# Kernel tuning notes

Hardware: AMD Instinct MI355X
Metric: run time of the kernel (lower is better)

## Reference

```python
import jax, jax.numpy as jnp
import numpy as np

B, L, D, H, DEPTH = 64, 384, 128, 8, 6
DH = D // H          # 16
VOCAB = 32000
C_OUT = 128
FF = 4 * D           # reformer_pytorch default ff_mult=4
SELF_VAL = -5e4      # TOKEN_SELF_ATTN_VALUE
MASK_VAL = -1e9      # causal mask value


def layer_norm(x, g, b, eps=1e-5):
    mu = jnp.mean(x, -1, keepdims=True)
    var = jnp.mean((x - mu) ** 2, -1, keepdims=True)
    return (x - mu) * jax.lax.rsqrt(var + eps) * g + b


def attn_block(x, p):
    # PreNorm + LSHSelfAttention in full-QK-attention fallback (seq <= full_attn_thres)
    h = layer_norm(x, p['ln1_g'], p['ln1_b'])
    qk = (h @ p['Wqk']).reshape(B, L, H, DH).transpose(0, 2, 1, 3)  # [B,H,L,DH]
    v = (h @ p['Wv']).reshape(B, L, H, DH).transpose(0, 2, 1, 3)
    # shared QK: q = qk, k = l2-normalized qk
    k = qk / jnp.maximum(jnp.linalg.norm(qk, axis=-1, keepdims=True), 1e-12)
    dots = jnp.einsum('bhid,bhjd->bhij', qk, k) * (DH ** -0.5)
    i = jnp.arange(L)
    eye = i[:, None] == i[None, :]
    future = i[None, :] > i[:, None]
    dots = jnp.where(eye, SELF_VAL, dots)   # token cannot (easily) attend to itself
    dots = jnp.where(future, MASK_VAL, dots)  # causal
    a = jax.nn.softmax(dots, axis=-1)
    o = jnp.einsum('bhij,bhjd->bhid', a, v).transpose(0, 2, 1, 3).reshape(B, L, D)
    return o @ p['Wo'] + p['bo']


def ff_block(x, p):
    h = layer_norm(x, p['ln2_g'], p['ln2_b'])
    h = jax.nn.gelu(h @ p['W1'] + p['b1'], approximate=False)
    return h @ p['W2'] + p['b2']


def forward(x_enc, emb, pos1, pos2, ln1_g, ln1_b, Wqk, Wv, Wo, bo,
            ln2_g, ln2_b, W1, b1, W2, b2, lnf_g, lnf_b, Wp, bp):
    # axial positional embedding (summed mode): (25,D) + (25,D) -> (625,D)
    pos = (pos1[:, None, :] + pos2[None, :, :]).reshape(25 * 25, D)[:L]
    x = emb[x_enc] + pos  # [B,L,D]

    layer_params = dict(ln1_g=ln1_g, ln1_b=ln1_b, Wqk=Wqk, Wv=Wv, Wo=Wo, bo=bo,
                        ln2_g=ln2_g, ln2_b=ln2_b, W1=W1, b1=b1, W2=W2, b2=b2)

    def block(carry, p):
        x1, x2 = carry
        y1 = x1 + attn_block(x2, p)
        y2 = x2 + ff_block(y1, p)
        return (y1, y2), None

    # reversible-net math: duplicate stream, run blocks, average the two halves
    (x1, x2), _ = jax.lax.scan(block, (x, x), layer_params)
    x = layer_norm((x1 + x2) * 0.5, lnf_g, lnf_b)
    return x.reshape(B, L * D) @ Wp + bp  # [B, C_OUT]


def setup_inputs() -> dict:
    key = jax.random.key(0)
    ks = jax.random.split(key, 12)
    s = 0.02
    inp = {
        'x_enc': jax.random.randint(ks[0], (B, L), 0, VOCAB, dtype=jnp.int32),
        'emb': jax.random.normal(ks[1], (VOCAB, D), jnp.float32) * s,
        'pos1': jax.random.normal(ks[2], (25, D), jnp.float32) * s,
        'pos2': jax.random.normal(ks[3], (25, D), jnp.float32) * s,
        'ln1_g': jnp.ones((DEPTH, D), jnp.float32),
        'ln1_b': jnp.zeros((DEPTH, D), jnp.float32),
        'Wqk': jax.random.normal(ks[4], (DEPTH, D, D), jnp.float32) * s,
        'Wv': jax.random.normal(ks[5], (DEPTH, D, D), jnp.float32) * s,
        'Wo': jax.random.normal(ks[6], (DEPTH, D, D), jnp.float32) * s,
        'bo': jnp.zeros((DEPTH, D), jnp.float32),
        'ln2_g': jnp.ones((DEPTH, D), jnp.float32),
        'ln2_b': jnp.zeros((DEPTH, D), jnp.float32),
        'W1': jax.random.normal(ks[7], (DEPTH, D, FF), jnp.float32) * s,
        'b1': jnp.zeros((DEPTH, FF), jnp.float32),
        'W2': jax.random.normal(ks[8], (DEPTH, FF, D), jnp.float32) * s,
        'b2': jnp.zeros((DEPTH, D), jnp.float32),
        'lnf_g': jnp.ones((D,), jnp.float32),
        'lnf_b': jnp.zeros((D,), jnp.float32),
        'Wp': jax.random.normal(ks[9], (L * D, C_OUT), jnp.float32) * s,
        'bp': jnp.zeros((C_OUT,), jnp.float32),
    }
    return inp


def reference(x_enc, emb, pos1, pos2, ln1_g, ln1_b, Wqk, Wv, Wo, bo,
              ln2_g, ln2_b, W1, b1, W2, b2, lnf_g, lnf_b, Wp, bp):
    return forward(x_enc, emb, pos1, pos2, ln1_g, ln1_b, Wqk, Wv, Wo, bo,
                   ln2_g, ln2_b, W1, b1, W2, b2, lnf_g, lnf_b, Wp, bp)
```

## Files before the change

### kernel.cpp

```cpp
#include <hip/hip_runtime.h>
#include <hip/hip_bf16.h>
#include <math.h>

#define BB 64
#define LL 384
#define DD 128
#define HH 8
#define DHH 16
#define DEPTH 6
#define FFD 512
#define MROWS (BB*LL)
#define COUT 128
#define KP (LL*DD)
#define KSPLIT 96
#define KCHUNK 512

typedef short bf16x8 __attribute__((ext_vector_type(8)));
typedef float f32x4 __attribute__((ext_vector_type(4)));

__device__ __forceinline__ unsigned short f2bs(float x) {
    __hip_bfloat16 h = __float2bfloat16(x);
    return *reinterpret_cast<unsigned short*>(&h);
}
__device__ __forceinline__ float bs2f(unsigned short u) {
    unsigned int v = ((unsigned int)u) << 16;
    return __uint_as_float(v);
}
__device__ __forceinline__ float gelu_exact(float x) {
    return 0.5f * x * (1.0f + erff(x * 0.70710678118654752f));
}

__global__ __launch_bounds__(256) void embedln_kernel(
    const int* __restrict__ x_enc, const float* __restrict__ emb,
    const float* __restrict__ pos1, const float* __restrict__ pos2,
    const float* __restrict__ g, const float* __restrict__ b,
    float* __restrict__ x1, float* __restrict__ x2,
    __hip_bfloat16* __restrict__ y)
{
    int wave = threadIdx.x >> 6;
    int lane = threadIdx.x & 63;
    int row = blockIdx.x * 4 + wave;
    int l = row % LL;
    int tok = x_enc[row];
    float2 e  = ((const float2*)(emb + (size_t)tok * DD))[lane];
    float2 p1 = ((const float2*)(pos1 + (l / 25) * DD))[lane];
    float2 p2 = ((const float2*)(pos2 + (l % 25) * DD))[lane];
    float2 v = make_float2(e.x + p1.x + p2.x, e.y + p1.y + p2.y);
    ((float2*)(x1 + (size_t)row * DD))[lane] = v;
    ((float2*)(x2 + (size_t)row * DD))[lane] = v;
    float2 gg = ((const float2*)g)[lane];
    float2 bb = ((const float2*)b)[lane];
    float s = v.x + v.y;
    float sq = v.x * v.x + v.y * v.y;
    #pragma unroll
    for (int off = 32; off > 0; off >>= 1) {
        s += __shfl_down(s, off, 64);
        sq += __shfl_down(sq, off, 64);
    }
    s = __shfl(s, 0, 64);
    sq = __shfl(sq, 0, 64);
    float mean = s * (1.0f / DD);
    float var = sq * (1.0f / DD) - mean * mean;
    float rstd = rsqrtf(var + 1e-5f);
    __hip_bfloat16* yp = y + (size_t)row * DD + lane * 2;
    yp[0] = __float2bfloat16((v.x - mean) * rstd * gg.x + bb.x);
    yp[1] = __float2bfloat16((v.y - mean) * rstd * gg.y + bb.y);
}

__device__ __forceinline__ void castT_body(
    const float* __restrict__ s, __hip_bfloat16* __restrict__ d,
    int K, int N, int kb, int nb)
{
    __shared__ float tile[32][33];
    int tx = threadIdx.x & 31, ty = threadIdx.x >> 5;
    #pragma unroll
    for (int r = 0; r < 32; r += 8)
        tile[r + ty][tx] = s[(size_t)(kb + r + ty) * N + nb + tx];
    __syncthreads();
    #pragma unroll
    for (int r = 0; r < 32; r += 8)
        d[(size_t)(nb + r + ty) * K + kb + tx] = __float2bfloat16(tile[tx][r + ty]);
}

__global__ __launch_bounds__(256) void cast_all_kernel(
    const float* __restrict__ Wqk, const float* __restrict__ Wv,
    const float* __restrict__ Wo,  const float* __restrict__ W1,
    const float* __restrict__ W2,
    __hip_bfloat16* __restrict__ dqk, __hip_bfloat16* __restrict__ dv,
    __hip_bfloat16* __restrict__ dwo, __hip_bfloat16* __restrict__ d1,
    __hip_bfloat16* __restrict__ d2)
{
    int z = blockIdx.x;
    if (z < 288) {
        int m = z >> 4, t = z & 15;
        int which = m / 6, dd = m % 6;
        const float* s = (which == 0 ? Wqk : (which == 1 ? Wv : Wo)) + (size_t)dd * 16384;
        __hip_bfloat16* d = (which == 0 ? dqk : (which == 1 ? dv : dwo))
                            + (size_t)dd * (which == 2 ? 16384 : 32768);
        castT_body(s, d, 128, 128, (t >> 2) * 32, (t & 3) * 32);
    } else if (z < 672) {
        int i = z - 288; int dd = i >> 6; int t = i & 63;
        castT_body(W1 + (size_t)dd * 65536, d1 + (size_t)dd * 65536,
                   128, 512, (t >> 4) * 32, (t & 15) * 32);
    } else {
        int i = z - 672; int dd = i >> 6; int t = i & 63;
        castT_body(W2 + (size_t)dd * 65536, d2 + (size_t)dd * 65536,
                   512, 128, (t >> 2) * 32, (t & 3) * 32);
    }
}

__global__ __launch_bounds__(256) void castWp_kernel(
    const float* __restrict__ src, __hip_bfloat16* __restrict__ dst)
{
    castT_body(src, dst, KP, 128, blockIdx.x * 32, blockIdx.y * 32);
}

template<int K, int N>
__global__ __launch_bounds__(256) void gemm_qkv_kernel(
    const __hip_bfloat16* __restrict__ A, const __hip_bfloat16* __restrict__ Bt,
    __hip_bfloat16* __restrict__ Cdst)
{
    __shared__ unsigned short As[64 * 128];
    __shared__ unsigned short Bs[128 * 128];
    int tid = threadIdx.x;
    int l = tid & 63, w = tid >> 6;
    int wr = w >> 1, wc = w & 1;
    int lr = l & 15, q = l >> 4;
    int m0 = blockIdx.y * 64;
    int n0 = blockIdx.x * 128;

    f32x4 acc[2][4];
    #pragma unroll
    for (int mt = 0; mt < 2; ++mt)
        #pragma unroll
        for (int nt = 0; nt < 4; ++nt) acc[mt][nt] = (f32x4){0.f, 0.f, 0.f, 0.f};

    for (int kt = 0; kt < K; kt += 128) {
        if (kt) __syncthreads();
        #pragma unroll
        for (int p = 0; p < 4; ++p) {
            int n = p * 256 + tid;
            int r = n >> 4;
            int c = (n & 15) ^ (r & 7);
            *(uint4*)&As[n * 8] = *(const uint4*)(A + (size_t)(m0 + r) * K + kt + c * 8);
        }
        #pragma unroll
        for (int p = 0; p < 8; ++p) {
            int n = p * 256 + tid;
            int r = n >> 4;
            int c = (n & 15) ^ (r & 7);
            *(uint4*)&Bs[n * 8] = *(const uint4*)(Bt + (size_t)(n0 + r) * K + kt + c * 8);
        }
        __syncthreads();
        #pragma unroll
        for (int kk = 0; kk < 4; ++kk) {
            bf16x8 afr[2], bfr[4];
            #pragma unroll
            for (int mt = 0; mt < 2; ++mt) {
                int rA = wr * 32 + mt * 16 + lr;
                int cc = (kk * 4 + q) ^ (rA & 7);
                afr[mt] = *(const bf16x8*)&As[(rA * 16 + cc) * 8];
            }
            #pragma unroll
            for (int nt = 0; nt < 4; ++nt) {
                int rB = wc * 64 + nt * 16 + lr;
                int cc = (kk * 4 + q) ^ (rB & 7);
                bfr[nt] = *(const bf16x8*)&Bs[(rB * 16 + cc) * 8];
            }
            #pragma unroll
            for (int mt = 0; mt < 2; ++mt)
                #pragma unroll
                for (int nt = 0; nt < 4; ++nt)
                    acc[mt][nt] = __builtin_amdgcn_mfma_f32_16x16x32_bf16(
                        afr[mt], bfr[nt], acc[mt][nt], 0, 0, 0);
        }
    }

    #pragma unroll
    for (int mt = 0; mt < 2; ++mt)
        #pragma unroll
        for (int nt = 0; nt < 4; ++nt) {
            int col = n0 + wc * 64 + nt * 16 + lr;
            #pragma unroll
            for (int r = 0; r < 4; ++r) {
                int row = m0 + wr * 32 + mt * 16 + q * 4 + r;
                Cdst[(size_t)row * N + col] = __float2bfloat16(acc[mt][nt][r]);
            }
        }
}

__global__ __launch_bounds__(256) void attn_kernel(
    const __hip_bfloat16* __restrict__ qkv, __hip_bfloat16* __restrict__ o)
{
    int z  = blockIdx.x >> 9;
    int bh = blockIdx.x & 511;
    int b = bh >> 3, hh = bh & 7;
    const unsigned short* base = (const unsigned short*)qkv + (size_t)b * LL * 256 + hh * DHH;

    __shared__ unsigned short knb[LL + 2][24];
    __shared__ unsigned short vtb[16][LL + 24];
    __shared__ float cq[LL];
    __shared__ unsigned short ptile[4][16][40];

    int t = threadIdx.x;
    for (int r = t; r < LL; r += 256) {
        const unsigned short* qp = base + (size_t)r * 256;
        unsigned short qs[16], vs16[16];
        *(uint4*)&qs[0]  = *(const uint4*)(qp);
        *(uint4*)&qs[8]  = *(const uint4*)(qp + 8);
        *(uint4*)&vs16[0] = *(const uint4*)(qp + 128);
        *(uint4*)&vs16[8] = *(const uint4*)(qp + 136);
        float q[16];
        #pragma unroll
        for (int d = 0; d < 16; ++d) q[d] = bs2f(qs[d]);
        float nrm = 0.f;
        #pragma unroll
        for (int d = 0; d < 16; ++d) nrm = fmaf(q[d], q[d], nrm);
        float qn = sqrtf(nrm);
        float inv = 1.0f / fmaxf(qn, 1e-12f);
        cq[r] = 0.25f * qn;
        unsigned short kb[16];
        #pragma unroll
        for (int d = 0; d < 16; ++d) kb[d] = f2bs(q[d] * inv);
        *(uint4*)&knb[r][0] = *(uint4*)&kb[0];
        *(uint4*)&knb[r][8] = *(uint4*)&kb[8];
        *(uint4*)&knb[r][16] = make_uint4(0u, 0u, 0u, 0u);
        #pragma unroll
        for (int d = 0; d < 16; ++d) vtb[d][r] = vs16[d];
    }
    if (t < 16) {
        #pragma unroll
        for (int c = 0; c < 24; ++c) vtb[t][LL + c] = 0;
    }
    if (t < 2) {
        #pragma unroll
        for (int c = 0; c < 24; ++c) knb[LL + t][c] = 0;
    }

    int w = t >> 6, l = t & 63;
    int lr = l & 15, q4 = l >> 4;
    __syncthreads();

    bf16x8 zfrag = {0, 0, 0, 0, 0, 0, 0, 0};
    bf16x8 onesf;
    #pragma unroll
    for (int i = 0; i < 8; ++i) onesf[i] = (short)0x3F80;

    int slot = 2 * w + z;
    int strips[3] = { slot, 15 - slot, 16 + slot };
    #pragma unroll
    for (int si = 0; si < 3; ++si) {
        int s = strips[si];
        int r0 = s * 16;
        bf16x8 bq = *(const bf16x8*)&knb[r0 + lr][q4 * 8];
        float ccq = cq[r0 + lr];
        int qg = r0 + lr;

        f32x4 oacc = (f32x4){0.f, 0.f, 0.f, 0.f};
        f32x4 lacc = (f32x4){0.f, 0.f, 0.f, 0.f};

        for (int jt = 0; jt <= s; jt += 2) {
            bf16x8 a0 = *(const bf16x8*)&knb[jt * 16 + lr][(q4 & 1) * 8];
            a0 = (q4 < 2) ? a0 : zfrag;
            bf16x8 a1 = *(const bf16x8*)&knb[(jt + 1) * 16 + lr][(q4 & 1) * 8];
            a1 = (q4 < 2) ? a1 : zfrag;
            f32x4 s0 = __builtin_amdgcn_mfma_f32_16x16x32_bf16(
                a0, bq, (f32x4){0.f, 0.f, 0.f, 0.f}, 0, 0, 0);
            f32x4 s1 = __builtin_amdgcn_mfma_f32_16x16x32_bf16(
                a1, bq, (f32x4){0.f, 0.f, 0.f, 0.f}, 0, 0, 0);

            unsigned int pk0[2], pk1[2];
            #pragma unroll
            for (int h = 0; h < 2; ++h) {
                int ja = jt * 16 + q4 * 4 + 2 * h;
                float pa = __expf(fmaf(s0[2 * h],     ccq, -ccq));
                pa = (ja < qg) ? pa : 0.f;
                float pb = __expf(fmaf(s0[2 * h + 1], ccq, -ccq));
                pb = (ja + 1 < qg) ? pb : 0.f;
                pk0[h] = (unsigned int)f2bs(pa) | ((unsigned int)f2bs(pb) << 16);
                float pc = __expf(fmaf(s1[2 * h],     ccq, -ccq));
                pc = (ja + 16 < qg) ? pc : 0.f;
                float pd = __expf(fmaf(s1[2 * h + 1], ccq, -ccq));
                pd = (ja + 17 < qg) ? pd : 0.f;
                pk1[h] = (unsigned int)f2bs(pc) | ((unsigned int)f2bs(pd) << 16);
            }
            *(uint2*)&ptile[w][lr][q4 * 4]      = make_uint2(pk0[0], pk0[1]);
            *(uint2*)&ptile[w][lr][16 + q4 * 4] = make_uint2(pk1[0], pk1[1]);
            asm volatile("s_waitcnt lgkmcnt(0)" ::: "memory");
            bf16x8 pfrag = *(const bf16x8*)&ptile[w][lr][q4 * 8];
            bf16x8 vfrag = *(const bf16x8*)&vtb[lr][jt * 16 + q4 * 8];
            oacc = __builtin_amdgcn_mfma_f32_16x16x32_bf16(pfrag, vfrag, oacc, 0, 0, 0);
            lacc = __builtin_amdgcn_mfma_f32_16x16x32_bf16(pfrag, onesf, lacc, 0, 0, 0);
        }

        if (s == 0 && q4 == 0) {
            lacc[0] = 1.0f;
            oacc[0] = bs2f(vtb[lr][0]);
        }
        unsigned short* ob = (unsigned short*)o + (size_t)(b * LL + r0) * DD + hh * 16 + lr;
        #pragma unroll
        for (int reg = 0; reg < 4; ++reg) {
            float ov = oacc[reg] / lacc[reg];
            ob[(size_t)(q4 * 4 + reg) * DD] = f2bs(ov);
        }
    }
}

__global__ __launch_bounds__(256) void mega_wolf_kernel(
    const __hip_bfloat16* __restrict__ Ao, const __hip_bfloat16* __restrict__ WoTd,
    const float* __restrict__ bod, float* __restrict__ x1,
    const float* __restrict__ lng, const float* __restrict__ lnb,
    const __hip_bfloat16* __restrict__ W1Td, const float* __restrict__ b1d,
    __hip_bfloat16* __restrict__ hff)
{
    __shared__ unsigned short As[32 * 128];
    __shared__ unsigned short Bs[128 * 128];
    int tid = threadIdx.x;
    int l = tid & 63, w = tid >> 6;
    int lr = l & 15, q = l >> 4;
    int m0 = blockIdx.x * 32;

    f32x4 acc[2][2];
    #pragma unroll
    for (int mt = 0; mt < 2; ++mt)
        #pragma unroll
        for (int nt = 0; nt < 2; ++nt) acc[mt][nt] = (f32x4){0.f, 0.f, 0.f, 0.f};

    #pragma unroll
    for (int p = 0; p < 2; ++p) {
        int n = p * 256 + tid;
        int r = n >> 4;
        int c = (n & 15) ^ (r & 7);
        *(uint4*)&As[n * 8] = *(const uint4*)(Ao + (size_t)(m0 + r) * 128 + c * 8);
    }
    #pragma unroll
    for (int p = 0; p < 8; ++p) {
        int n = p * 256 + tid;
        int r = n >> 4;
        int c = (n & 15) ^ (r & 7);
        *(uint4*)&Bs[n * 8] = *(const uint4*)(WoTd + (size_t)r * 128 + c * 8);
    }
    __syncthreads();
    #pragma unroll
    for (int kk = 0; kk < 4; ++kk) {
        bf16x8 afr[2], bfr[2];
        #pragma unroll
        for (int mt = 0; mt < 2; ++mt) {
            int rA = mt * 16 + lr;
            int cc = (kk * 4 + q) ^ (rA & 7);
            afr[mt] = *(const bf16x8*)&As[(rA * 16 + cc) * 8];
        }
        #pragma unroll
        for (int nt = 0; nt < 2; ++nt) {
            int rB = w * 32 + nt * 16 + lr;
            int cc = (kk * 4 + q) ^ (rB & 7);
            bfr[nt] = *(const bf16x8*)&Bs[(rB * 16 + cc) * 8];
        }
        #pragma unroll
        for (int mt = 0; mt < 2; ++mt)
            #pragma unroll
            for (int nt = 0; nt < 2; ++nt)
                acc[mt][nt] = __builtin_amdgcn_mfma_f32_16x16x32_bf16(
                    afr[mt], bfr[nt], acc[mt][nt], 0, 0, 0);
    }

    float* fp = (float*)Bs;
    __syncthreads();
    #pragma unroll
    for (int mt = 0; mt < 2; ++mt)
        #pragma unroll
        for (int nt = 0; nt < 2; ++nt) {
            int col = w * 32 + nt * 16 + lr;
            float bv = bod[col];
            #pragma unroll
            for (int r = 0; r < 4; ++r) {
                int rowL = mt * 16 + q * 4 + r;
                fp[rowL * 128 + col] = acc[mt][nt][r] + bv
                                       + x1[(size_t)(m0 + rowL) * 128 + col];
            }
        }
    __syncthreads();
    {
        int rl = tid >> 3, sub = tid & 7;
        float s = 0.f, sq = 0.f;
        #pragma unroll
        for (int c4 = 0; c4 < 4; ++c4) {
            float4 v = *(const float4*)&fp[rl * 128 + sub * 16 + c4 * 4];
            s  += (v.x + v.y) + (v.z + v.w);
            sq += (v.x * v.x + v.y * v.y) + (v.z * v.z + v.w * v.w);
        }
        s  += __shfl_xor(s, 1);  s  += __shfl_xor(s, 2);  s  += __shfl_xor(s, 4);
        sq += __shfl_xor(sq, 1); sq += __shfl_xor(sq, 2); sq += __shfl_xor(sq, 4);
        float mean = s * (1.0f / 128.0f);
        float var  = sq * (1.0f / 128.0f) - mean * mean;
        float rstd = rsqrtf(var + 1e-5f);
        #pragma unroll
        for (int c4 = 0; c4 < 4; ++c4) {
            int col = sub * 16 + c4 * 4;
            float4 v  = *(const float4*)&fp[rl * 128 + col];
            *(float4*)(x1 + (size_t)(m0 + rl) * 128 + col) = v;
            float4 g4 = *(const float4*)(lng + col);
            float4 b4 = *(const float4*)(lnb + col);
            unsigned short pk[4];
            pk[0] = f2bs((v.x - mean) * rstd * g4.x + b4.x);
            pk[1] = f2bs((v.y - mean) * rstd * g4.y + b4.y);
            pk[2] = f2bs((v.z - mean) * rstd * g4.z + b4.z);
            pk[3] = f2bs((v.w - mean) * rstd * g4.w + b4.w);
            int addr = rl * 128 + (((col >> 3) ^ (rl & 7)) << 3) + (col & 7);
            *(ushort4*)&As[addr] = *(ushort4*)&pk[0];
        }
    }
    __syncthreads();

    for (int nc = 0; nc < 4; ++nc) {
        if (nc) __syncthreads();
        #pragma unroll
        for (int p = 0; p < 8; ++p) {
            int n = p * 256 + tid;
            int r = n >> 4;
            int c = (n & 15) ^ (r & 7);
            *(uint4*)&Bs[n * 8] = *(const uint4*)(W1Td + (size_t)(nc * 128 + r) * 128 + c * 8);
        }
        __syncthreads();
        f32x4 a2[2][2];
        #pragma unroll
        for (int mt = 0; mt < 2; ++mt)
            #pragma unroll
            for (int nt = 0; nt < 2; ++nt) a2[mt][nt] = (f32x4){0.f, 0.f, 0.f, 0.f};
        #pragma unroll
        for (int kk = 0; kk < 4; ++kk) {
            bf16x8 afr[2], bfr[2];
            #pragma unroll
            for (int mt = 0; mt < 2; ++mt) {
                int rA = mt * 16 + lr;
                int cc = (kk * 4 + q) ^ (rA & 7);
                afr[mt] = *(const bf16x8*)&As[(rA * 16 + cc) * 8];
            }
            #pragma unroll
            for (int nt = 0; nt < 2; ++nt) {
                int rB = w * 32 + nt * 16 + lr;
                int cc = (kk * 4 + q) ^ (rB & 7);
                bfr[nt] = *(const bf16x8*)&Bs[(rB * 16 + cc) * 8];
            }
            #pragma unroll
            for (int mt = 0; mt < 2; ++mt)
                #pragma unroll
                for (int nt = 0; nt < 2; ++nt)
                    a2[mt][nt] = __builtin_amdgcn_mfma_f32_16x16x32_bf16(
                        afr[mt], bfr[nt], a2[mt][nt], 0, 0, 0);
        }
        #pragma unroll
        for (int mt = 0; mt < 2; ++mt)
            #pragma unroll
            for (int nt = 0; nt < 2; ++nt) {
                int colg = nc * 128 + w * 32 + nt * 16 + lr;
                float bv = b1d[colg];
                #pragma unroll
                for (int r = 0; r < 4; ++r) {
                    int row = m0 + mt * 16 + q * 4 + r;
                    hff[(size_t)row * 512 + colg] =
                        __float2bfloat16(gelu_exact(a2[mt][nt][r] + bv));
                }
            }
    }
}

template<bool LAST>
__global__ __launch_bounds__(256) void mega_ffq_kernel(
    const __hip_bfloat16* __restrict__ Ahff, const __hip_bfloat16* __restrict__ W2Td,
    const float* __restrict__ b2d, float* __restrict__ x2,
    const float* __restrict__ x1,
    const float* __restrict__ lng, const float* __restrict__ lnb,
    const __hip_bfloat16* __restrict__ WqvTd, __hip_bfloat16* __restrict__ qkv,
    __hip_bfloat16* __restrict__ hout)
{
    __shared__ unsigned short As[32 * 128];
    __shared__ unsigned short Bs[128 * 128];
    int tid = threadIdx.x;
    int l = tid & 63, w = tid >> 6;
    int lr = l & 15, q = l >> 4;
    int m0 = blockIdx.x * 32;

    f32x4 acc[2][2];
    #pragma unroll
    for (int mt = 0; mt < 2; ++mt)
        #pragma unroll
        for (int nt = 0; nt < 2; ++nt) acc[mt][nt] = (f32x4){0.f, 0.f, 0.f, 0.f};

    for (int kt = 0; kt < 512; kt += 128) {
        if (kt) __syncthreads();
        #pragma unroll
        for (int p = 0; p < 2; ++p) {
            int n = p * 256 + tid;
            int r = n >> 4;
            int c = (n & 15) ^ (r & 7);
            *(uint4*)&As[n * 8] = *(const uint4*)(Ahff + (size_t)(m0 + r) * 512 + kt + c * 8);
        }
        #pragma unroll
        for (int p = 0; p < 8; ++p) {
            int n = p * 256 + tid;
            int r = n >> 4;
            int c = (n & 15) ^ (r & 7);
            *(uint4*)&Bs[n * 8] = *(const uint4*)(W2Td + (size_t)r * 512 + kt + c * 8);
        }
        __syncthreads();
        #pragma unroll
        for (int kk = 0; kk < 4; ++kk) {
            bf16x8 afr[2], bfr[2];
            #pragma unroll
            for (int mt = 0; mt < 2; ++mt) {
                int rA = mt * 16 + lr;
                int cc = (kk * 4 + q) ^ (rA & 7);
                afr[mt] = *(const bf16x8*)&As[(rA * 16 + cc) * 8];
            }
            #pragma unroll
            for (int nt = 0; nt < 2; ++nt) {
                int rB = w * 32 + nt * 16 + lr;
                int cc = (kk * 4 + q) ^ (rB & 7);
                bfr[nt] = *(const bf16x8*)&Bs[(rB * 16 + cc) * 8];
            }
            #pragma unroll
            for (int mt = 0; mt < 2; ++mt)
                #pragma unroll
                for (int nt = 0; nt < 2; ++nt)
                    acc[mt][nt] = __builtin_amdgcn_mfma_f32_16x16x32_bf16(
                        afr[mt], bfr[nt], acc[mt][nt], 0, 0, 0);
        }
    }

    float* fp = (float*)Bs;
    __syncthreads();
    #pragma unroll
    for (int mt = 0; mt < 2; ++mt)
        #pragma unroll
        for (int nt = 0; nt < 2; ++nt) {
            int col = w * 32 + nt * 16 + lr;
            float bv = b2d[col];
            #pragma unroll
            for (int r = 0; r < 4; ++r) {
                int rowL = mt * 16 + q * 4 + r;
                fp[rowL * 128 + col] = acc[mt][nt][r] + bv
                                       + x2[(size_t)(m0 + rowL) * 128 + col];
            }
        }
    __syncthreads();
    {
        int rl = tid >> 3, sub = tid & 7;
        float s = 0.f, sq = 0.f;
        #pragma unroll
        for (int c4 = 0; c4 < 4; ++c4) {
            float4 v = *(const float4*)&fp[rl * 128 + sub * 16 + c4 * 4];
            if (LAST) {
                float4 xo = *(const float4*)(x1 + (size_t)(m0 + rl) * 128 + sub * 16 + c4 * 4);
                v.x = (v.x + xo.x) * 0.5f; v.y = (v.y + xo.y) * 0.5f;
                v.z = (v.z + xo.z) * 0.5f; v.w = (v.w + xo.w) * 0.5f;
            }
            s  += (v.x + v.y) + (v.z + v.w);
            sq += (v.x * v.x + v.y * v.y) + (v.z * v.z + v.w * v.w);
        }
        s  += __shfl_xor(s, 1);  s  += __shfl_xor(s, 2);  s  += __shfl_xor(s, 4);
        sq += __shfl_xor(sq, 1); sq += __shfl_xor(sq, 2); sq += __shfl_xor(sq, 4);
        float mean = s * (1.0f / 128.0f);
        float var  = sq * (1.0f / 128.0f) - mean * mean;
        float rstd = rsqrtf(var + 1e-5f);
        #pragma unroll
        for (int c4 = 0; c4 < 4; ++c4) {
            int col = sub * 16 + c4 * 4;
            float4 v = *(const float4*)&fp[rl * 128 + col];
            if (LAST) {
                float4 xo = *(const float4*)(x1 + (size_t)(m0 + rl) * 128 + col);
                v.x = (v.x + xo.x) * 0.5f; v.y = (v.y + xo.y) * 0.5f;
                v.z = (v.z + xo.z) * 0.5f; v.w = (v.w + xo.w) * 0.5f;
            } else {
                *(float4*)(x2 + (size_t)(m0 + rl) * 128 + col) = v;
            }
            float4 g4 = *(const float4*)(lng + col);
            float4 b4 = *(const float4*)(lnb + col);
            unsigned short pk[4];
            pk[0] = f2bs((v.x - mean) * rstd * g4.x + b4.x);
            pk[1] = f2bs((v.y - mean) * rstd * g4.y + b4.y);
            pk[2] = f2bs((v.z - mean) * rstd * g4.z + b4.z);
            pk[3] = f2bs((v.w - mean) * rstd * g4.w + b4.w);
            if (LAST) {
                *(ushort4*)((unsigned short*)hout + (size_t)(m0 + rl) * 128 + col)
                    = *(ushort4*)&pk[0];
            } else {
                int addr = rl * 128 + (((col >> 3) ^ (rl & 7)) << 3) + (col & 7);
                *(ushort4*)&As[addr] = *(ushort4*)&pk[0];
            }
        }
    }
    __syncthreads();

    if (!LAST) {
        for (int nc = 0; nc < 2; ++nc) {
            if (nc) __syncthreads();
            #pragma unroll
            for (int p = 0; p < 8; ++p) {
                int n = p * 256 + tid;
                int r = n >> 4;
                int c = (n & 15) ^ (r & 7);
                *(uint4*)&Bs[n * 8] = *(const uint4*)(WqvTd + (size_t)(nc * 128 + r) * 128 + c * 8);
            }
            __syncthreads();
            f32x4 a2[2][2];
            #pragma unroll
            for (int mt = 0; mt < 2; ++mt)
                #pragma unroll
                for (int nt = 0; nt < 2; ++nt) a2[mt][nt] = (f32x4){0.f, 0.f, 0.f, 0.f};
            #pragma unroll
            for (int kk = 0; kk < 4; ++kk) {
                bf16x8 afr[2], bfr[2];
                #pragma unroll
                for (int mt = 0; mt < 2; ++mt) {
                    int rA = mt * 16 + lr;
                    int cc = (kk * 4 + q) ^ (rA & 7);
                    afr[mt] = *(const bf16x8*)&As[(rA * 16 + cc) * 8];
                }
                #pragma unroll
                for (int nt = 0; nt < 2; ++nt) {
                    int rB = w * 32 + nt * 16 + lr;
                    int cc = (kk * 4 + q) ^ (rB & 7);
                    bfr[nt] = *(const bf16x8*)&Bs[(rB * 16 + cc) * 8];
                }
                #pragma unroll
                for (int mt = 0; mt < 2; ++mt)
                    #pragma unroll
                    for (int nt = 0; nt < 2; ++nt)
                        a2[mt][nt] = __builtin_amdgcn_mfma_f32_16x16x32_bf16(
                            afr[mt], bfr[nt], a2[mt][nt], 0, 0, 0);
            }
            #pragma unroll
            for (int mt = 0; mt < 2; ++mt)
                #pragma unroll
                for (int nt = 0; nt < 2; ++nt) {
                    int colg = nc * 128 + w * 32 + nt * 16 + lr;
                    #pragma unroll
                    for (int r = 0; r < 4; ++r) {
                        int row = m0 + mt * 16 + q * 4 + r;
                        qkv[(size_t)row * 256 + colg] = __float2bfloat16(a2[mt][nt][r]);
                    }
                }
        }
    }
}

__global__ __launch_bounds__(256) void final_mfma_kernel(
    const __hip_bfloat16* __restrict__ A, const __hip_bfloat16* __restrict__ Bt,
    float* __restrict__ partials)
{
    __shared__ unsigned short As[64 * 128];
    __shared__ unsigned short Bs[128 * 128];
    int tid = threadIdx.x;
    int l = tid & 63, w = tid >> 6;
    int wr = w >> 1, wc = w & 1;
    int lr = l & 15, q = l >> 4;
    int kbase = blockIdx.x * KCHUNK;

    f32x4 acc[2][4];
    #pragma unroll
    for (int mt = 0; mt < 2; ++mt)
        #pragma unroll
        for (int nt = 0; nt < 4; ++nt) acc[mt][nt] = (f32x4){0.f, 0.f, 0.f, 0.f};

    for (int kt = 0; kt < KCHUNK; kt += 128) {
        if (kt) __syncthreads();
        #pragma unroll
        for (int p = 0; p < 4; ++p) {
            int n = p * 256 + tid;
            int r = n >> 4;
            int c = (n & 15) ^ (r & 7);
            *(uint4*)&As[n * 8] = *(const uint4*)(A + (size_t)r * KP + kbase + kt + c * 8);
        }
        #pragma unroll
        for (int p = 0; p < 8; ++p) {
            int n = p * 256 + tid;
            int r = n >> 4;
            int c = (n & 15) ^ (r & 7);
            *(uint4*)&Bs[n * 8] = *(const uint4*)(Bt + (size_t)r * KP + kbase + kt + c * 8);
        }
        __syncthreads();
        #pragma unroll
        for (int kk = 0; kk < 4; ++kk) {
            bf16x8 afr[2], bfr[4];
            #pragma unroll
            for (int mt = 0; mt < 2; ++mt) {
                int rA = wr * 32 + mt * 16 + lr;
                int cc = (kk * 4 + q) ^ (rA & 7);
                afr[mt] = *(const bf16x8*)&As[(rA * 16 + cc) * 8];
            }
            #pragma unroll
            for (int nt = 0; nt < 4; ++nt) {
                int rB = wc * 64 + nt * 16 + lr;
                int cc = (kk * 4 + q) ^ (rB & 7);
                bfr[nt] = *(const bf16x8*)&Bs[(rB * 16 + cc) * 8];
            }
            #pragma unroll
            for (int mt = 0; mt < 2; ++mt)
                #pragma unroll
                for (int nt = 0; nt < 4; ++nt)
                    acc[mt][nt] = __builtin_amdgcn_mfma_f32_16x16x32_bf16(
                        afr[mt], bfr[nt], acc[mt][nt], 0, 0, 0);
        }
    }

    float* dst = partials + (size_t)blockIdx.x * (64 * 128);
    #pragma unroll
    for (int mt = 0; mt < 2; ++mt)
        #pragma unroll
        for (int nt = 0; nt < 4; ++nt) {
            int col = wc * 64 + nt * 16 + lr;
            #pragma unroll
            for (int r = 0; r < 4; ++r) {
                int row = wr * 32 + mt * 16 + q * 4 + r;
                dst[row * 128 + col] = acc[mt][nt][r];
            }
        }
}

__global__ __launch_bounds__(256) void final_reduce_kernel(
    const float* __restrict__ partials, const float* __restrict__ bp,
    float* __restrict__ out)
{
    int j = blockIdx.x * 256 + threadIdx.x;
    float s = bp[j & (COUT - 1)];
    #pragma unroll 8
    for (int p = 0; p < KSPLIT; ++p)
        s += partials[(size_t)p * 8192 + j];
    out[j] = s;
}

extern "C" void kernel_launch(void* const* d_in, const int* in_sizes, int n_in,
                              void* d_out, int out_size, void* d_ws, size_t ws_size,
                              hipStream_t stream)
{
    const int*   x_enc = (const int*)  d_in[0];
    const float* emb   = (const float*)d_in[1];
    const float* pos1  = (const float*)d_in[2];
    const float* pos2  = (const float*)d_in[3];
    const float* ln1_g = (const float*)d_in[4];
    const float* ln1_b = (const float*)d_in[5];
    const float* Wqk   = (const float*)d_in[6];
    const float* Wv    = (const float*)d_in[7];
    const float* Wo    = (const float*)d_in[8];
    const float* bo    = (const float*)d_in[9];
    const float* ln2_g = (const float*)d_in[10];
    const float* ln2_b = (const float*)d_in[11];
    const float* W1    = (const float*)d_in[12];
    const float* b1    = (const float*)d_in[13];
    const float* W2    = (const float*)d_in[14];
    const float* b2    = (const float*)d_in[15];
    const float* lnf_g = (const float*)d_in[16];
    const float* lnf_b = (const float*)d_in[17];
    const float* Wp    = (const float*)d_in[18];
    const float* bp    = (const float*)d_in[19];
    float* out = (float*)d_out;

    const size_t SZ = (size_t)MROWS * DD;
    float* ws_f = (float*)d_ws;
    float* x1 = ws_f;
    float* x2 = ws_f + SZ;
    __hip_bfloat16* hff  = (__hip_bfloat16*)(ws_f + 2 * SZ);
    __hip_bfloat16* h_bf = (__hip_bfloat16*)(ws_f + 4 * SZ);
    __hip_bfloat16* o_bf = h_bf + SZ;
    __hip_bfloat16* wqvT = o_bf + SZ;
    __hip_bfloat16* woT  = wqvT + 6 * 32768;
    __hip_bfloat16* w1T  = woT  + 6 * 16384;
    __hip_bfloat16* w2T  = w1T  + 6 * 65536;
    __hip_bfloat16* WpT  = w2T  + 6 * 65536;
    __hip_bfloat16* qkv  = WpT;
    float* partials = (float*)(WpT + (size_t)COUT * KP);

    cast_all_kernel<<<dim3(1056), dim3(256), 0, stream>>>(
        Wqk, Wv, Wo, W1, W2, wqvT, wqvT + 16384, woT, w1T, w2T);
    embedln_kernel<<<dim3(MROWS / 4), dim3(256), 0, stream>>>(
        x_enc, emb, pos1, pos2, ln1_g, ln1_b, x1, x2, h_bf);
    gemm_qkv_kernel<128, 256><<<dim3(2, MROWS / 64), dim3(256), 0, stream>>>(
        h_bf, wqvT, qkv);

    for (int d = 0; d < DEPTH; ++d) {
        attn_kernel<<<dim3(BB * HH * 2), dim3(256), 0, stream>>>(qkv, o_bf);
        mega_wolf_kernel<<<dim3(MROWS / 32), dim3(256), 0, stream>>>(
            o_bf, woT + (size_t)d * 16384, bo + d * DD, x1,
            ln2_g + d * DD, ln2_b + d * DD,
            w1T + (size_t)d * 65536, b1 + d * FFD, hff);
        if (d < DEPTH - 1) {
            mega_ffq_kernel<false><<<dim3(MROWS / 32), dim3(256), 0, stream>>>(
                hff, w2T + (size_t)d * 65536, b2 + d * DD, x2, nullptr,
                ln1_g + (d + 1) * DD, ln1_b + (d + 1) * DD,
                wqvT + (size_t)(d + 1) * 32768, qkv, nullptr);
        } else {
            mega_ffq_kernel<true><<<dim3(MROWS / 32), dim3(256), 0, stream>>>(
                hff, w2T + (size_t)d * 65536, b2 + d * DD, x2, x1,
                lnf_g, lnf_b, nullptr, nullptr, h_bf);
        }
    }

    castWp_kernel<<<dim3(KP / 32, 4), dim3(256), 0, stream>>>(Wp, WpT);
    final_mfma_kernel<<<dim3(KSPLIT), dim3(256), 0, stream>>>(h_bf, WpT, partials);
    final_reduce_kernel<<<dim3(32), dim3(256), 0, stream>>>(partials, bp, out);
}
```

Measured before the change: 555.0 us.

## Fuse FF1-GELU-FF2 and next-layer QKV into single per-layer kernel

Merges the Wo+LN2+W1+GELU kernel with the W2+residual+LN1+QKV kernel. The 512-wide GELU activation for a 32-row tile now lives in shared memory one 128-column chunk at a time, and W2 partial products accumulate in registers. This removes the global write and re-read of the large bf16 hff buffer and one launch per layer. In exchange it adds an extra shared-memory buffer, which may lower occupancy, and more barriers inside the chunk loop.

```diff
diff --git a/kernel.cpp b/kernel.cpp
--- a/kernel.cpp
+++ b/kernel.cpp
@@ -306,15 +306,21 @@
     }
 }
 
-__global__ __launch_bounds__(256) void mega_wolf_kernel(
+template<bool LAST>
+__global__ __launch_bounds__(256) void mega_layer_kernel(
     const __hip_bfloat16* __restrict__ Ao, const __hip_bfloat16* __restrict__ WoTd,
     const float* __restrict__ bod, float* __restrict__ x1,
-    const float* __restrict__ lng, const float* __restrict__ lnb,
+    const float* __restrict__ ln2g, const float* __restrict__ ln2b,
     const __hip_bfloat16* __restrict__ W1Td, const float* __restrict__ b1d,
-    __hip_bfloat16* __restrict__ hff)
+    const __hip_bfloat16* __restrict__ W2Td, const float* __restrict__ b2d,
+    float* __restrict__ x2,
+    const float* __restrict__ ln1g, const float* __restrict__ ln1b,
+    const __hip_bfloat16* __restrict__ WqvTd, __hip_bfloat16* __restrict__ qkv,
+    __hip_bfloat16* __restrict__ hout)
 {
     __shared__ unsigned short As[32 * 128];
     __shared__ unsigned short Bs[128 * 128];
+    __shared__ unsigned short Hs[32 * 128];
     int tid = threadIdx.x;
     int l = tid & 63, w = tid >> 6;
     int lr = l & 15, q = l >> 4;
@@ -399,18 +405,24 @@
             int col = sub * 16 + c4 * 4;
             float4 v  = *(const float4*)&fp[rl * 128 + col];
             *(float4*)(x1 + (size_t)(m0 + rl) * 128 + col) = v;
-            float4 g4 = *(const float4*)(lng + col);
-            float4 b4 = *(const float4*)(lnb + col);
+            float4 g4 = *(const float4*)(ln2g + col);
+            float4 b4 = *(const float4*)(ln2b + col);
             unsigned short pk[4];
             pk[0] = f2bs((v.x - mean) * rstd * g4.x + b4.x);
             pk[1] = f2bs((v.y - mean) * rstd * g4.y + b4.y);
             pk[2] = f2bs((v.z - mean) * rstd * g4.z + b4.z);
             pk[3] = f2bs((v.w - mean) * rstd * g4.w + b4.w);
             int addr = rl * 128 + (((col >> 3) ^ (rl & 7)) << 3) + (col & 7);
-            *(ushort4*)&As[addr] = *(ushort4*)&pk[0];
-        }
-    }
-    __syncthreads();
+            *(ushort4*)&Hs[addr] = *(ushort4*)&pk[0];
+        }
+    }
+    __syncthreads();
+
+    f32x4 ffacc[2][2];
+    #pragma unroll
+    for (int mt = 0; mt < 2; ++mt)
+        #pragma unroll
+        for (int nt = 0; nt < 2; ++nt) ffacc[mt][nt] = (f32x4){0.f, 0.f, 0.f, 0.f};
 
     for (int nc = 0; nc < 4; ++nc) {
         if (nc) __syncthreads();
@@ -422,11 +434,55 @@
             *(uint4*)&Bs[n * 8] = *(const uint4*)(W1Td + (size_t)(nc * 128 + r) * 128 + c * 8);
         }
         __syncthreads();
-        f32x4 a2[2][2];
+        f32x4 a1[2][2];
         #pragma unroll
         for (int mt = 0; mt < 2; ++mt)
             #pragma unroll
-            for (int nt = 0; nt < 2; ++nt) a2[mt][nt] = (f32x4){0.f, 0.f, 0.f, 0.f};
+            for (int nt = 0; nt < 2; ++nt) a1[mt][nt] = (f32x4){0.f, 0.f, 0.f, 0.f};
+        #pragma unroll
+        for (int kk = 0; kk < 4; ++kk) {
+            bf16x8 afr[2], bfr[2];
+            #pragma unroll
+            for (int mt = 0; mt < 2; ++mt) {
+                int rA = mt * 16 + lr;
+                int cc = (kk * 4 + q) ^ (rA & 7);
+                afr[mt] = *(const bf16x8*)&Hs[(rA * 16 + cc) * 8];
+            }
+            #pragma unroll
+            for (int nt = 0; nt < 2; ++nt) {
+                int rB = w * 32 + nt * 16 + lr;
+                int cc = (kk * 4 + q) ^ (rB & 7);
+                bfr[nt] = *(const bf16x8*)&Bs[(rB * 16 + cc) * 8];
+            }
+            #pragma unroll
+            for (int mt = 0; mt < 2; ++mt)
+                #pragma unroll
+                for (int nt = 0; nt < 2; ++nt)
+                    a1[mt][nt] = __builtin_amdgcn_mfma_f32_16x16x32_bf16(
+                        afr[mt], bfr[nt], a1[mt][nt], 0, 0, 0);
+        }
+        #pragma unroll
+        for (int mt = 0; mt < 2; ++mt)
+            #pragma unroll
+            for (int nt = 0; nt < 2; ++nt) {
+                int k = w * 32 + nt * 16 + lr;
+                float bv = b1d[nc * 128 + k];
+                #pragma unroll
+                for (int r = 0; r < 4; ++r) {
+                    int row = mt * 16 + q * 4 + r;
+                    int addr = row * 128 + (((k >> 3) ^ (row & 7)) << 3) + (k & 7);
+                    As[addr] = f2bs(gelu_exact(a1[mt][nt][r] + bv));
+                }
+            }
+        __syncthreads();
+        #pragma unroll
+        for (int p = 0; p < 8; ++p) {
+            int n = p * 256 + tid;
+            int r = n >> 4;
+            int c = (n & 15) ^ (r & 7);
+            *(uint4*)&Bs[n * 8] = *(const uint4*)(W2Td + (size_t)r * 512 + nc * 128 + c * 8);
+        }
+        __syncthreads();
         #pragma unroll
         for (int kk = 0; kk < 4; ++kk) {
             bf16x8 afr[2], bfr[2];
@@ -446,89 +502,11 @@
             for (int mt = 0; mt < 2; ++mt)
                 #pragma unroll
                 for (int nt = 0; nt < 2; ++nt)
-                    a2[mt][nt] = __builtin_amdgcn_mfma_f32_16x16x32_bf16(
-                        afr[mt], bfr[nt], a2[mt][nt], 0, 0, 0);
-        }
-        #pragma unroll
-        for (int mt = 0; mt < 2; ++mt)
-            #pragma unroll
-            for (int nt = 0; nt < 2; ++nt) {
-                int colg = nc * 128 + w * 32 + nt * 16 + lr;
-                float bv = b1d[colg];
-                #pragma unroll
-                for (int r = 0; r < 4; ++r) {
-                    int row = m0 + mt * 16 + q * 4 + r;
-                    hff[(size_t)row * 512 + colg] =
-                        __float2bfloat16(gelu_exact(a2[mt][nt][r] + bv));
-                }
-            }
-    }
-}
-
-template<bool LAST>
-__global__ __launch_bounds__(256) void mega_ffq_kernel(
-    const __hip_bfloat16* __restrict__ Ahff, const __hip_bfloat16* __restrict__ W2Td,
-    const float* __restrict__ b2d, float* __restrict__ x2,
-    const float* __restrict__ x1,
-    const float* __restrict__ lng, const float* __restrict__ lnb,
-    const __hip_bfloat16* __restrict__ WqvTd, __hip_bfloat16* __restrict__ qkv,
-    __hip_bfloat16* __restrict__ hout)
-{
-    __shared__ unsigned short As[32 * 128];
-    __shared__ unsigned short Bs[128 * 128];
-    int tid = threadIdx.x;
-    int l = tid & 63, w = tid >> 6;
-    int lr = l & 15, q = l >> 4;
-    int m0 = blockIdx.x * 32;
-
-    f32x4 acc[2][2];
-    #pragma unroll
-    for (int mt = 0; mt < 2; ++mt)
-        #pragma unroll
-        for (int nt = 0; nt < 2; ++nt) acc[mt][nt] = (f32x4){0.f, 0.f, 0.f, 0.f};
-
-    for (int kt = 0; kt < 512; kt += 128) {
-        if (kt) __syncthreads();
-        #pragma unroll
-        for (int p = 0; p < 2; ++p) {
-            int n = p * 256 + tid;
-            int r = n >> 4;
-            int c = (n & 15) ^ (r & 7);
-            *(uint4*)&As[n * 8] = *(const uint4*)(Ahff + (size_t)(m0 + r) * 512 + kt + c * 8);
-        }
-        #pragma unroll
-        for (int p = 0; p < 8; ++p) {
-            int n = p * 256 + tid;
-            int r = n >> 4;
-            int c = (n & 15) ^ (r & 7);
-            *(uint4*)&Bs[n * 8] = *(const uint4*)(W2Td + (size_t)r * 512 + kt + c * 8);
-        }
-        __syncthreads();
-        #pragma unroll
-        for (int kk = 0; kk < 4; ++kk) {
-            bf16x8 afr[2], bfr[2];
-            #pragma unroll
-            for (int mt = 0; mt < 2; ++mt) {
-                int rA = mt * 16 + lr;
-                int cc = (kk * 4 + q) ^ (rA & 7);
-                afr[mt] = *(const bf16x8*)&As[(rA * 16 + cc) * 8];
-            }
-            #pragma unroll
-            for (int nt = 0; nt < 2; ++nt) {
-                int rB = w * 32 + nt * 16 + lr;
-                int cc = (kk * 4 + q) ^ (rB & 7);
-                bfr[nt] = *(const bf16x8*)&Bs[(rB * 16 + cc) * 8];
-            }
-            #pragma unroll
-            for (int mt = 0; mt < 2; ++mt)
-                #pragma unroll
-                for (int nt = 0; nt < 2; ++nt)
-                    acc[mt][nt] = __builtin_amdgcn_mfma_f32_16x16x32_bf16(
-                        afr[mt], bfr[nt], acc[mt][nt], 0, 0, 0);
-        }
-    }
-
-    float* fp = (float*)Bs;
+                    ffacc[mt][nt] = __builtin_amdgcn_mfma_f32_16x16x32_bf16(
+                        afr[mt], bfr[nt], ffacc[mt][nt], 0, 0, 0);
+        }
+    }
+
     __syncthreads();
     #pragma unroll
     for (int mt = 0; mt < 2; ++mt)
@@ -539,7 +517,7 @@
             #pragma unroll
             for (int r = 0; r < 4; ++r) {
                 int rowL = mt * 16 + q * 4 + r;
-                fp[rowL * 128 + col] = acc[mt][nt][r] + bv
+                fp[rowL * 128 + col] = ffacc[mt][nt][r] + bv
                                        + x2[(size_t)(m0 + rowL) * 128 + col];
             }
         }
@@ -574,8 +552,8 @@
             } else {
                 *(float4*)(x2 + (size_t)(m0 + rl) * 128 + col) = v;
             }
-            float4 g4 = *(const float4*)(lng + col);
-            float4 b4 = *(const float4*)(lnb + col);
+            float4 g4 = *(const float4*)(ln1g + col);
+            float4 b4 = *(const float4*)(ln1b + col);
             unsigned short pk[4];
             pk[0] = f2bs((v.x - mean) * rstd * g4.x + b4.x);
             pk[1] = f2bs((v.y - mean) * rstd * g4.y + b4.y);
@@ -586,7 +564,7 @@
                     = *(ushort4*)&pk[0];
             } else {
                 int addr = rl * 128 + (((col >> 3) ^ (rl & 7)) << 3) + (col & 7);
-                *(ushort4*)&As[addr] = *(ushort4*)&pk[0];
+                *(ushort4*)&Hs[addr] = *(ushort4*)&pk[0];
             }
         }
     }
@@ -615,7 +593,7 @@
                 for (int mt = 0; mt < 2; ++mt) {
                     int rA = mt * 16 + lr;
                     int cc = (kk * 4 + q) ^ (rA & 7);
-                    afr[mt] = *(const bf16x8*)&As[(rA * 16 + cc) * 8];
+                    afr[mt] = *(const bf16x8*)&Hs[(rA * 16 + cc) * 8];
                 }
                 #pragma unroll
                 for (int nt = 0; nt < 2; ++nt) {
@@ -760,8 +738,7 @@
     float* ws_f = (float*)d_ws;
     float* x1 = ws_f;
     float* x2 = ws_f + SZ;
-    __hip_bfloat16* hff  = (__hip_bfloat16*)(ws_f + 2 * SZ);
-    __hip_bfloat16* h_bf = (__hip_bfloat16*)(ws_f + 4 * SZ);
+    __hip_bfloat16* h_bf = (__hip_bfloat16*)(ws_f + 2 * SZ);
     __hip_bfloat16* o_bf = h_bf + SZ;
     __hip_bfloat16* wqvT = o_bf + SZ;
     __hip_bfloat16* woT  = wqvT + 6 * 32768;
@@ -780,18 +757,20 @@
 
     for (int d = 0; d < DEPTH; ++d) {
         attn_kernel<<<dim3(BB * HH * 2), dim3(256), 0, stream>>>(qkv, o_bf);
-        mega_wolf_kernel<<<dim3(MROWS / 32), dim3(256), 0, stream>>>(
-            o_bf, woT + (size_t)d * 16384, bo + d * DD, x1,
-            ln2_g + d * DD, ln2_b + d * DD,
-            w1T + (size_t)d * 65536, b1 + d * FFD, hff);
         if (d < DEPTH - 1) {
-            mega_ffq_kernel<false><<<dim3(MROWS / 32), dim3(256), 0, stream>>>(
-                hff, w2T + (size_t)d * 65536, b2 + d * DD, x2, nullptr,
+            mega_layer_kernel<false><<<dim3(MROWS / 32), dim3(256), 0, stream>>>(
+                o_bf, woT + (size_t)d * 16384, bo + d * DD, x1,
+                ln2_g + d * DD, ln2_b + d * DD,
+                w1T + (size_t)d * 65536, b1 + d * FFD,
+                w2T + (size_t)d * 65536, b2 + d * DD, x2,
                 ln1_g + (d + 1) * DD, ln1_b + (d + 1) * DD,
                 wqvT + (size_t)(d + 1) * 32768, qkv, nullptr);
         } else {
-            mega_ffq_kernel<true><<<dim3(MROWS / 32), dim3(256), 0, stream>>>(
-                hff, w2T + (size_t)d * 65536, b2 + d * DD, x2, x1,
+            mega_layer_kernel<true><<<dim3(MROWS / 32), dim3(256), 0, stream>>>(
+                o_bf, woT + (size_t)d * 16384, bo + d * DD, x1,
+                ln2_g + d * DD, ln2_b + d * DD,
+                w1T + (size_t)d * 65536, b1 + d * FFD,
+                w2T + (size_t)d * 65536, b2 + d * DD, x2,
                 lnf_g, lnf_b, nullptr, nullptr, h_bf);
         }
     }
```

New measurement: 586.7 us. +5.7%, slower.
